# Kernel tuning notes

Measured on AMD Instinct MI355X. Metric: run time of the kernel, lower is better.

## Reference

```python
import jax, jax.numpy as jnp
import numpy as np


def setup_inputs() -> dict:
    key = jax.random.key(0)
    k1, k2, k3, k4 = jax.random.split(key, 4)
    bs, n, f_in, f_out, n_head = 4, 2048, 64, 64, 8
    h = jax.random.normal(k1, (bs, n, f_in), dtype=jnp.float32)
    adj = jnp.ones((bs, n, n), dtype=bool)  # accepted by forward but unused
    # xavier-uniform-like init scales
    w = jax.random.uniform(k2, (n_head, f_in, f_out), dtype=jnp.float32,
                           minval=-1.0, maxval=1.0) * np.sqrt(6.0 / (f_in + f_out))
    a_src = jax.random.uniform(k3, (n_head, f_out, 1), dtype=jnp.float32,
                               minval=-1.0, maxval=1.0) * np.sqrt(6.0 / (f_out + 1))
    a_dst = jax.random.uniform(k4, (n_head, f_out, 1), dtype=jnp.float32,
                               minval=-1.0, maxval=1.0) * np.sqrt(6.0 / (f_out + 1))
    bias_p = jnp.zeros((f_out,), dtype=jnp.float32)
    return {"h": h, "adj": adj, "w": w, "a_src": a_src, "a_dst": a_dst, "bias_p": bias_p}


def reference(h, adj, w, a_src, a_dst, bias_p):
    # h: [b, n, f_in], w: [h, f_in, f_out]
    h_prime = jnp.einsum('bnf,hfo->bhno', h, w)          # [b, h, n, f_out]
    t = jnp.tanh(h_prime)
    attn_src = jnp.einsum('bhno,ho->bhn', t, a_src[..., 0])  # [b, h, n]
    attn_dst = jnp.einsum('bhno,ho->bhn', t, a_dst[..., 0])  # [b, h, n]
    # attn[b,h,i,j] = src[b,h,i] + dst[b,h,j]  (dense; adj unused in original)
    attn = attn_src[..., :, None] + attn_dst[..., None, :]   # [b, h, n, n]
    attn = jnp.where(attn >= 0, attn, 0.2 * attn)            # leaky_relu(0.2)
    attn = jax.nn.softmax(attn, axis=-1)
    # dropout p=0.0 -> identity
    out = jnp.einsum('bhij,bhjo->bhio', attn, h_prime)       # [b, h, n, f_out]
    return out + bias_p
```

## Files before the change

### kernel.cpp

```cpp
#include <hip/hip_runtime.h>
#include <hip/hip_bf16.h>

#define NN 2048
#define FF 64
#define NH 8
#define BDIM 4
#define BH 32

typedef __attribute__((ext_vector_type(8))) short short8;
typedef __attribute__((ext_vector_type(4))) float floatx4;
typedef __attribute__((ext_vector_type(4))) unsigned uint4v;

__device__ __forceinline__ float LDIN(const void* p, size_t i, int b16) {
    return b16 ? __bfloat162float(((const __hip_bfloat16*)p)[i]) : ((const float*)p)[i];
}
__device__ __forceinline__ unsigned packhi(float f0, float f1) {
    return __builtin_amdgcn_perm(__float_as_uint(f1), __float_as_uint(f0), 0x07060302);
}
__device__ __forceinline__ float hitrunc(float x) {
    return __uint_as_float(__float_as_uint(x) & 0xFFFF0000u);
}
__device__ __forceinline__ ushort bf16bits(float v) {
    __hip_bfloat16 b = __float2bfloat16(v);
    return __builtin_bit_cast(ushort, b);
}
__device__ __forceinline__ int SWZ(int row, int col) {
    return row * 64 + ((((col >> 3) ^ (row & 7)) << 3) | (col & 7));
}
__device__ __forceinline__ float fast_tanh(float v) {
    float ex = __expf(2.0f * v);
    return 1.0f - 2.0f * __builtin_amdgcn_rcpf(ex + 1.0f);
}
__device__ __forceinline__ int sniff_b16(const void* h) {
    unsigned word = ((const unsigned*)h)[threadIdx.x & 63];
    unsigned lowexp = (word >> 7) & 0xFFu;
    bool plaus = (lowexp >= 96u && lowexp <= 159u);
    unsigned long long m = __ballot(plaus);
    return (__popcll(m) >= 48) ? 1 : 0;
}

__global__ __launch_bounds__(256) void k_prep(
    const void* __restrict__ h, const void* __restrict__ w,
    ushort* __restrict__ wF, int* __restrict__ flagOut)
{
    const int hd = blockIdx.x, t = threadIdx.x;
    __shared__ int sb16;
    if (t < 64) {
        int f = sniff_b16(h);
        if (t == 0) { sb16 = f; if (hd == 0) flagOut[0] = f; }
    }
    __syncthreads();
    const int b16 = sb16;

#pragma unroll
    for (int g = 0; g < 2; ++g) {
        int gi = t * 2 + g;
        int ml = gi & 15, q = (gi >> 4) & 3, kc = (gi >> 6) & 1, nt = (gi >> 7) & 3;
        int n = nt * 16 + ml, kb = kc * 32 + q * 8;
        size_t off = (size_t)hd * 4096 + ((nt * 2 + kc) * 4 + q) * 128 + ml * 8;
        if (b16) {
            const ushort* wp = (const ushort*)w + (size_t)hd * FF * FF;
            ushort hi[8];
#pragma unroll
            for (int j = 0; j < 8; ++j) hi[j] = wp[(kb + j) * FF + n];
            *(uint4v*)&wF[off] = __builtin_bit_cast(uint4v, *(short8*)hi);
            short8 z = {0, 0, 0, 0, 0, 0, 0, 0};
            *(uint4v*)&wF[off + 32768] = __builtin_bit_cast(uint4v, z);
        } else {
            const float* wp = (const float*)w + (size_t)hd * FF * FF;
            float x[8];
#pragma unroll
            for (int j = 0; j < 8; ++j) x[j] = wp[(kb + j) * FF + n];
            uint4v hv = { packhi(x[0], x[1]), packhi(x[2], x[3]),
                          packhi(x[4], x[5]), packhi(x[6], x[7]) };
            uint4v lv = { packhi(x[0] - hitrunc(x[0]), x[1] - hitrunc(x[1])),
                          packhi(x[2] - hitrunc(x[2]), x[3] - hitrunc(x[3])),
                          packhi(x[4] - hitrunc(x[4]), x[5] - hitrunc(x[5])),
                          packhi(x[6] - hitrunc(x[6]), x[7] - hitrunc(x[7])) };
            *(uint4v*)&wF[off] = hv;
            *(uint4v*)&wF[off + 32768] = lv;
        }
    }
}

__global__ __launch_bounds__(256) void k_proj(
    const void* __restrict__ h, const ushort* __restrict__ wF,
    const void* __restrict__ asrc, const void* __restrict__ adst,
    ushort* __restrict__ hpTt, float* __restrict__ rArr,
    float* __restrict__ edHa, float* __restrict__ edLa)
{
    const int t  = threadIdx.x;
    const int rt = blockIdx.x & 31;
    const int hd = (blockIdx.x >> 5) & 7;
    const int b  = blockIdx.x >> 8;
    const int bh = b * NH + hd;
    const int r0 = rt * 64;

    __shared__ int sb16;
    __shared__ ushort aHi[64 * 64];
    __shared__ ushort aLo[64 * 64];
    __shared__ ushort trans[64 * 64];
    if (t < 64) {
        int f = sniff_b16(h);
        if (t == 0) sb16 = f;
    }
    __syncthreads();
    const int b16 = sb16;

    const int lane = t & 63, wv = t >> 6;
    const int ml = lane & 15, q = lane >> 4;

    if (b16) {
        const ushort* hsrc = (const ushort*)h + (size_t)(b * NN + r0) * FF;
#pragma unroll
        for (int g0 = 0; g0 < 2; ++g0) {
            int g = t + g0 * 256;
            int row = g >> 3, c8 = (g & 7) * 8;
            uint4v u = *(const uint4v*)(hsrc + row * FF + c8);
            *(uint4v*)&aHi[SWZ(row, c8)] = u;
        }
    } else {
        const float* hsrc = (const float*)h + (size_t)(b * NN + r0) * FF;
#pragma unroll
        for (int g0 = 0; g0 < 4; ++g0) {
            int g = t + g0 * 256;
            int row = g >> 4, c4 = (g & 15) * 4;
            floatx4 x = *(const floatx4*)(hsrc + row * FF + c4);
            uint2 hi2 = { packhi(x[0], x[1]), packhi(x[2], x[3]) };
            uint2 lo2 = { packhi(x[0] - hitrunc(x[0]), x[1] - hitrunc(x[1])),
                          packhi(x[2] - hitrunc(x[2]), x[3] - hitrunc(x[3])) };
            *(uint2*)&aHi[SWZ(row, c4)] = hi2;
            *(uint2*)&aLo[SWZ(row, c4)] = lo2;
        }
    }
    __syncthreads();

    short8 ah[2], al[2];
#pragma unroll
    for (int kc = 0; kc < 2; ++kc) {
        ah[kc] = *(const short8*)&aHi[SWZ(wv * 16 + ml, kc * 32 + q * 8)];
        if (!b16) al[kc] = *(const short8*)&aLo[SWZ(wv * 16 + ml, kc * 32 + q * 8)];
    }
    short8 bhf[4][2], blf[4][2];
    const ushort* wfh = wF + (size_t)hd * 4096;
#pragma unroll
    for (int nt = 0; nt < 4; ++nt)
#pragma unroll
        for (int kc = 0; kc < 2; ++kc) {
            size_t off = ((nt * 2 + kc) * 4 + q) * 128 + ml * 8;
            bhf[nt][kc] = __builtin_bit_cast(short8, *(const uint4v*)&wfh[off]);
            if (!b16) blf[nt][kc] = __builtin_bit_cast(short8, *(const uint4v*)&wfh[off + 32768]);
        }

    float aS[4], aD[4];
#pragma unroll
    for (int nt = 0; nt < 4; ++nt) {
        aS[nt] = LDIN(asrc, hd * FF + nt * 16 + ml, b16);
        aD[nt] = LDIN(adst, hd * FF + nt * 16 + ml, b16);
    }

    floatx4 acc[4];
#pragma unroll
    for (int nt = 0; nt < 4; ++nt) {
        floatx4 a = {0.f, 0.f, 0.f, 0.f};
        if (b16) {
#pragma unroll
            for (int kc = 0; kc < 2; ++kc)
                a = __builtin_amdgcn_mfma_f32_16x16x32_bf16(ah[kc], bhf[nt][kc], a, 0, 0, 0);
        } else {
#pragma unroll
            for (int kc = 0; kc < 2; ++kc) {
                a = __builtin_amdgcn_mfma_f32_16x16x32_bf16(ah[kc], bhf[nt][kc], a, 0, 0, 0);
                a = __builtin_amdgcn_mfma_f32_16x16x32_bf16(ah[kc], blf[nt][kc], a, 0, 0, 0);
                a = __builtin_amdgcn_mfma_f32_16x16x32_bf16(al[kc], bhf[nt][kc], a, 0, 0, 0);
            }
        }
        acc[nt] = a;
    }

#pragma unroll
    for (int nt = 0; nt < 4; ++nt) {
        ushort b0 = bf16bits(acc[nt][0]), b1 = bf16bits(acc[nt][1]);
        ushort b2 = bf16bits(acc[nt][2]), b3 = bf16bits(acc[nt][3]);
        uint2 pk = { (unsigned)b0 | ((unsigned)b1 << 16),
                     (unsigned)b2 | ((unsigned)b3 << 16) };
        *(uint2*)&trans[SWZ(nt * 16 + ml, wv * 16 + q * 4)] = pk;
    }

    float ps[4] = {0.f, 0.f, 0.f, 0.f}, pd[4] = {0.f, 0.f, 0.f, 0.f};
#pragma unroll
    for (int nt = 0; nt < 4; ++nt)
#pragma unroll
        for (int reg = 0; reg < 4; ++reg) {
            float tv = fast_tanh(acc[nt][reg]);
            ps[reg] += tv * aS[nt];
            pd[reg] += tv * aD[nt];
        }
#pragma unroll
    for (int msk = 1; msk < 16; msk <<= 1)
#pragma unroll
        for (int reg = 0; reg < 4; ++reg) {
            ps[reg] += __shfl_xor(ps[reg], msk, 64);
            pd[reg] += __shfl_xor(pd[reg], msk, 64);
        }
    if (ml == 0) {
#pragma unroll
        for (int reg = 0; reg < 4; ++reg) {
            int i = bh * NN + r0 + wv * 16 + q * 4 + reg;
            float sv = ps[reg], dv = pd[reg];
            rArr[i] = __expf(-0.8f * sv);
            edHa[i] = __expf(dv);
            edLa[i] = __expf(0.2f * dv);
        }
    }
    __syncthreads();
    {
        const int o = t >> 2, part = (t & 3) * 16;
        uint4v v0 = *(const uint4v*)&trans[SWZ(o, part)];
        uint4v v1 = *(const uint4v*)&trans[SWZ(o, part + 8)];
        ushort* dst = hpTt + (((size_t)bh * 32 + rt) * 64 + o) * 64 + part;
        *(uint4v*)dst = v0;
        *(uint4v*)(dst + 8) = v1;
    }
}

__global__ __launch_bounds__(512) void k_attn(
    const ushort* __restrict__ hpTt, const float* __restrict__ rArr,
    const float* __restrict__ edHa, const float* __restrict__ edLa,
    const void* __restrict__ bias, const int* __restrict__ flag,
    void* __restrict__ out)
{
    const int b16 = flag[0];
    const int t = threadIdx.x;
    const int wv = t >> 6, lane = t & 63;
    const int ml = lane & 15, q = lane >> 4;
    const int bh = blockIdx.x & 31;
    const int i0 = (blockIdx.x >> 5) * 128 + wv * 16;

    __shared__ ushort Bc[4][64 * 64];
    __shared__ __align__(16) float ehS[NN];
    __shared__ __align__(16) float elS[NN];

    ((floatx4*)ehS)[t] = ((const floatx4*)(edHa + bh * NN))[t];
    ((floatx4*)elS)[t] = ((const floatx4*)(edLa + bh * NN))[t];

    const ushort* src = hpTt + (size_t)bh * NN * FF;
    const float r = rArr[bh * NN + i0 + ml];

    const short8 ONESB = {0x3F80, 0x3F80, 0x3F80, 0x3F80,
                          0x3F80, 0x3F80, 0x3F80, 0x3F80};

    floatx4 acc[4];
#pragma unroll
    for (int nt = 0; nt < 4; ++nt) acc[nt] = (floatx4){0.f, 0.f, 0.f, 0.f};
    floatx4 accD = {0.f, 0.f, 0.f, 0.f};

    auto stage = [&](int c) {
        uint4v u = *(const uint4v*)(src + (size_t)c * 4096 + t * 8);
        *(uint4v*)&Bc[c & 3][SWZ(t >> 3, (t & 7) * 8)] = u;
    };

    auto compute = [&](int c) {
        const int j0 = c * 64, buf = c & 3;
#pragma unroll
        for (int ks = 0; ks < 2; ++ks) {
            const int col = ks * 32 + q * 8;
            floatx4 eh0 = *(const floatx4*)&ehS[j0 + col];
            floatx4 eh1 = *(const floatx4*)&ehS[j0 + col + 4];
            floatx4 el0 = *(const floatx4*)&elS[j0 + col];
            floatx4 el1 = *(const floatx4*)&elS[j0 + col + 4];
            short8 Bf[4];
#pragma unroll
            for (int nt = 0; nt < 4; ++nt)
                Bf[nt] = *(const short8*)&Bc[buf][SWZ(nt * 16 + ml, col)];
            float p[8];
#pragma unroll
            for (int j = 0; j < 4; ++j) {
                p[j]     = fmaxf(eh0[j], r * el0[j]);
                p[j + 4] = fmaxf(eh1[j], r * el1[j]);
            }
            uint4v hv = { packhi(p[0], p[1]), packhi(p[2], p[3]),
                          packhi(p[4], p[5]), packhi(p[6], p[7]) };
            short8 PH = __builtin_bit_cast(short8, hv);
#pragma unroll
            for (int nt = 0; nt < 4; ++nt)
                acc[nt] = __builtin_amdgcn_mfma_f32_16x16x32_bf16(PH, Bf[nt], acc[nt], 0, 0, 0);
            accD = __builtin_amdgcn_mfma_f32_16x16x32_bf16(PH, ONESB, accD, 0, 0, 0);
        }
    };

    stage(0); stage(1);
    __syncthreads();
    for (int c = 0; c < 32; c += 2) {
        if (c + 2 < 32) { stage(c + 2); stage(c + 3); }
        compute(c);
        compute(c + 1);
        __syncthreads();
    }

    float biasv[4];
#pragma unroll
    for (int nt = 0; nt < 4; ++nt) biasv[nt] = LDIN(bias, nt * 16 + ml, b16);

#pragma unroll
    for (int reg = 0; reg < 4; ++reg) {
        float inv = 1.0f / accD[reg];
        int i = i0 + q * 4 + reg;
#pragma unroll
        for (int nt = 0; nt < 4; ++nt) {
            float val = acc[nt][reg] * inv + biasv[nt];
            size_t oi = ((size_t)bh * NN + i) * FF + nt * 16 + ml;
            if (b16) ((__hip_bfloat16*)out)[oi] = __float2bfloat16(val);
            else     ((float*)out)[oi] = val;
        }
    }
}

extern "C" void kernel_launch(void* const* d_in, const int* in_sizes, int n_in,
                              void* d_out, int out_size, void* d_ws, size_t ws_size,
                              hipStream_t stream) {
    const void* h    = d_in[0];
    const void* w    = d_in[2];
    const void* asrc = d_in[3];
    const void* adst = d_in[4];
    const void* bias = d_in[5];

    float* ws = (float*)d_ws;
    int*    flag = (int*)ws;
    ushort* hpTt = (ushort*)(ws + 16);
    float*  rArr = (float*)(hpTt + (size_t)BH * NN * FF);
    float*  edHa = rArr + BH * NN;
    float*  edLa = edHa + BH * NN;
    ushort* wF   = (ushort*)(edLa + BH * NN);

    k_prep<<<NH, 256, 0, stream>>>(h, w, wF, flag);
    k_proj<<<BDIM * NH * 32, 256, 0, stream>>>(h, wF, asrc, adst,
                                               hpTt, rArr, edHa, edLa);
    k_attn<<<BH * 16, 512, 0, stream>>>(hpTt, rArr, edHa, edLa,
                                        bias, flag, d_out);
}
```

Baseline: 139.1 us.

## Replace dense attention matmul with sort plus prefix-sum formulation

```diff
diff --git a/kernel.cpp b/kernel.cpp
--- a/kernel.cpp
+++ b/kernel.cpp
@@ -19,10 +19,6 @@
 }
 __device__ __forceinline__ float hitrunc(float x) {
     return __uint_as_float(__float_as_uint(x) & 0xFFFF0000u);
-}
-__device__ __forceinline__ ushort bf16bits(float v) {
-    __hip_bfloat16 b = __float2bfloat16(v);
-    return __builtin_bit_cast(ushort, b);
 }
 __device__ __forceinline__ int SWZ(int row, int col) {
     return row * 64 + ((((col >> 3) ^ (row & 7)) << 3) | (col & 7));
@@ -37,6 +33,16 @@
     bool plaus = (lowexp >= 96u && lowexp <= 159u);
     unsigned long long m = __ballot(plaus);
     return (__popcll(m) >= 48) ? 1 : 0;
+}
+__device__ __forceinline__ unsigned long long packKey(float d, int j) {
+    unsigned u = __float_as_uint(d);
+    u = (u & 0x80000000u) ? ~u : (u | 0x80000000u);
+    return ((unsigned long long)(~u) << 32) | (unsigned)j;
+}
+__device__ __forceinline__ float unpackD(unsigned long long kk) {
+    unsigned u = ~(unsigned)(kk >> 32);
+    u = (u & 0x80000000u) ? (u & 0x7FFFFFFFu) : ~u;
+    return __uint_as_float(u);
 }
 
 __global__ __launch_bounds__(256) void k_prep(
@@ -86,8 +92,8 @@
 __global__ __launch_bounds__(256) void k_proj(
     const void* __restrict__ h, const ushort* __restrict__ wF,
     const void* __restrict__ asrc, const void* __restrict__ adst,
-    ushort* __restrict__ hpTt, float* __restrict__ rArr,
-    float* __restrict__ edHa, float* __restrict__ edLa)
+    float* __restrict__ hpF, float* __restrict__ sArr, float* __restrict__ dArr,
+    float* __restrict__ rArr)
 {
     const int t  = threadIdx.x;
     const int rt = blockIdx.x & 31;
@@ -99,7 +105,7 @@
     __shared__ int sb16;
     __shared__ ushort aHi[64 * 64];
     __shared__ ushort aLo[64 * 64];
-    __shared__ ushort trans[64 * 64];
+    __shared__ float  sF[64 * 68];
     if (t < 64) {
         int f = sniff_b16(h);
         if (t == 0) sb16 = f;
@@ -179,13 +185,10 @@
     }
 
 #pragma unroll
-    for (int nt = 0; nt < 4; ++nt) {
-        ushort b0 = bf16bits(acc[nt][0]), b1 = bf16bits(acc[nt][1]);
-        ushort b2 = bf16bits(acc[nt][2]), b3 = bf16bits(acc[nt][3]);
-        uint2 pk = { (unsigned)b0 | ((unsigned)b1 << 16),
-                     (unsigned)b2 | ((unsigned)b3 << 16) };
-        *(uint2*)&trans[SWZ(nt * 16 + ml, wv * 16 + q * 4)] = pk;
-    }
+    for (int nt = 0; nt < 4; ++nt)
+#pragma unroll
+        for (int reg = 0; reg < 4; ++reg)
+            sF[(wv * 16 + q * 4 + reg) * 68 + nt * 16 + ml] = acc[nt][reg];
 
     float ps[4] = {0.f, 0.f, 0.f, 0.f}, pd[4] = {0.f, 0.f, 0.f, 0.f};
 #pragma unroll
@@ -208,111 +211,175 @@
         for (int reg = 0; reg < 4; ++reg) {
             int i = bh * NN + r0 + wv * 16 + q * 4 + reg;
             float sv = ps[reg], dv = pd[reg];
+            sArr[i] = sv;
+            dArr[i] = dv;
             rArr[i] = __expf(-0.8f * sv);
-            edHa[i] = __expf(dv);
-            edLa[i] = __expf(0.2f * dv);
         }
     }
     __syncthreads();
     {
-        const int o = t >> 2, part = (t & 3) * 16;
-        uint4v v0 = *(const uint4v*)&trans[SWZ(o, part)];
-        uint4v v1 = *(const uint4v*)&trans[SWZ(o, part + 8)];
-        ushort* dst = hpTt + (((size_t)bh * 32 + rt) * 64 + o) * 64 + part;
-        *(uint4v*)dst = v0;
-        *(uint4v*)(dst + 8) = v1;
-    }
-}
-
-__global__ __launch_bounds__(512) void k_attn(
-    const ushort* __restrict__ hpTt, const float* __restrict__ rArr,
-    const float* __restrict__ edHa, const float* __restrict__ edLa,
+        const int row = t >> 2, cs = (t & 3) * 16;
+        const float* sp = &sF[row * 68 + cs];
+        float* dst = hpF + ((size_t)bh * NN + r0 + row) * 64 + cs;
+        *(floatx4*)(dst)      = *(const floatx4*)(sp);
+        *(floatx4*)(dst + 4)  = *(const floatx4*)(sp + 4);
+        *(floatx4*)(dst + 8)  = *(const floatx4*)(sp + 8);
+        *(floatx4*)(dst + 12) = *(const floatx4*)(sp + 12);
+    }
+}
+
+__global__ __launch_bounds__(1024) void k_mid(
+    const float* __restrict__ dArr, const float* __restrict__ hpF,
+    float* __restrict__ SD,
+    float* __restrict__ PreR, float* __restrict__ SufR,
+    float* __restrict__ PreS, float* __restrict__ SufS)
+{
+    const int bh = blockIdx.x, t = threadIdx.x;
+    const int lane = t & 63, wv = t >> 6;
+    __shared__ unsigned long long kp[2048];
+    __shared__ float Teh[64][64];
+    __shared__ float Tel[64][64];
+    __shared__ float TehS[64], TelS[64];
+
+    kp[t]        = packKey(dArr[bh * NN + t], t);
+    kp[t + 1024] = packKey(dArr[bh * NN + t + 1024], t + 1024);
+    __syncthreads();
+
+    for (int k = 2; k <= 2048; k <<= 1) {
+        for (int j = k >> 1; j > 0; j >>= 1) {
+#pragma unroll
+            for (int e = 0; e < 2; ++e) {
+                int a = t + e * 1024, b = a ^ j;
+                if (b > a) {
+                    unsigned long long ka = kp[a], kb = kp[b];
+                    bool up = ((a & k) == 0);
+                    if ((ka > kb) == up) { kp[a] = kb; kp[b] = ka; }
+                }
+            }
+            __syncthreads();
+        }
+    }
+
+    SD[bh * NN + t]        = unpackD(kp[t]);
+    SD[bh * NN + t + 1024] = unpackD(kp[t + 1024]);
+
+#pragma unroll
+    for (int cc = 0; cc < 4; ++cc) {
+        int c = wv * 4 + cc;
+        float teh = 0.f, tel = 0.f, tehs = 0.f, tels = 0.f;
+#pragma unroll 4
+        for (int u = 0; u < 32; ++u) {
+            unsigned long long kk = kp[c * 32 + u];
+            int jj = (int)(kk & 0xFFFFFFFFu);
+            float d = unpackD(kk);
+            float eh = __expf(d), el = __expf(0.2f * d);
+            float hv = hpF[((size_t)bh * NN + jj) * 64 + lane];
+            teh += eh * hv; tel += el * hv; tehs += eh; tels += el;
+        }
+        Teh[c][lane] = teh; Tel[c][lane] = tel;
+        if (lane == 0) { TehS[c] = tehs; TelS[c] = tels; }
+    }
+    __syncthreads();
+
+    if (wv == 0) {
+        float rp = 0.f, rps = 0.f;
+        for (int c = 0; c < 64; ++c) {
+            float tv = Teh[c][lane]; Teh[c][lane] = rp; rp += tv;
+            if (lane == 0) { float ts = TehS[c]; TehS[c] = rps; rps += ts; }
+        }
+        PreR[((size_t)bh * 2049 + 2048) * 64 + lane] = rp;
+        if (lane == 0) PreS[(size_t)bh * 2049 + 2048] = rps;
+    } else if (wv == 1) {
+        float rs = 0.f, rss = 0.f;
+        for (int c = 63; c >= 0; --c) {
+            float tv = Tel[c][lane]; Tel[c][lane] = rs; rs += tv;
+            if (lane == 0) { float ts = TelS[c]; TelS[c] = rss; rss += ts; }
+        }
+        SufR[((size_t)bh * 2049 + 2048) * 64 + lane] = 0.f;
+        if (lane == 0) SufS[(size_t)bh * 2049 + 2048] = 0.f;
+    }
+    __syncthreads();
+
+#pragma unroll
+    for (int cc = 0; cc < 4; ++cc) {
+        int c = wv * 4 + cc;
+        float run = Teh[c][lane];
+        float runs = TehS[c];
+#pragma unroll 4
+        for (int u = 0; u < 32; ++u) {
+            int x = c * 32 + u;
+            unsigned long long kk = kp[x];
+            int jj = (int)(kk & 0xFFFFFFFFu);
+            PreR[((size_t)bh * 2049 + x) * 64 + lane] = run;
+            if (lane == 0) PreS[(size_t)bh * 2049 + x] = runs;
+            float eh = __expf(unpackD(kk));
+            float hv = hpF[((size_t)bh * NN + jj) * 64 + lane];
+            run += eh * hv; runs += eh;
+        }
+        float runb = Tel[c][lane];
+        float runbs = TelS[c];
+#pragma unroll 4
+        for (int u = 31; u >= 0; --u) {
+            int x = c * 32 + u;
+            unsigned long long kk = kp[x];
+            int jj = (int)(kk & 0xFFFFFFFFu);
+            float el = __expf(0.2f * unpackD(kk));
+            float hv = hpF[((size_t)bh * NN + jj) * 64 + lane];
+            runb += el * hv; runbs += el;
+            SufR[((size_t)bh * 2049 + x) * 64 + lane] = runb;
+            if (lane == 0) SufS[(size_t)bh * 2049 + x] = runbs;
+        }
+    }
+}
+
+__global__ __launch_bounds__(128) void k_out(
+    const float* __restrict__ SD, const float* __restrict__ sArr,
+    const float* __restrict__ rArr,
+    const float* __restrict__ PreR, const float* __restrict__ SufR,
+    const float* __restrict__ PreS, const float* __restrict__ SufS,
     const void* __restrict__ bias, const int* __restrict__ flag,
     void* __restrict__ out)
 {
     const int b16 = flag[0];
     const int t = threadIdx.x;
+    const int bh = blockIdx.x >> 4;
+    const int i0 = (blockIdx.x & 15) * 128;
     const int wv = t >> 6, lane = t & 63;
-    const int ml = lane & 15, q = lane >> 4;
-    const int bh = blockIdx.x & 31;
-    const int i0 = (blockIdx.x >> 5) * 128 + wv * 16;
-
-    __shared__ ushort Bc[4][64 * 64];
-    __shared__ __align__(16) float ehS[NN];
-    __shared__ __align__(16) float elS[NN];
-
-    ((floatx4*)ehS)[t] = ((const floatx4*)(edHa + bh * NN))[t];
-    ((floatx4*)elS)[t] = ((const floatx4*)(edLa + bh * NN))[t];
-
-    const ushort* src = hpTt + (size_t)bh * NN * FF;
-    const float r = rArr[bh * NN + i0 + ml];
-
-    const short8 ONESB = {0x3F80, 0x3F80, 0x3F80, 0x3F80,
-                          0x3F80, 0x3F80, 0x3F80, 0x3F80};
-
-    floatx4 acc[4];
-#pragma unroll
-    for (int nt = 0; nt < 4; ++nt) acc[nt] = (floatx4){0.f, 0.f, 0.f, 0.f};
-    floatx4 accD = {0.f, 0.f, 0.f, 0.f};
-
-    auto stage = [&](int c) {
-        uint4v u = *(const uint4v*)(src + (size_t)c * 4096 + t * 8);
-        *(uint4v*)&Bc[c & 3][SWZ(t >> 3, (t & 7) * 8)] = u;
-    };
-
-    auto compute = [&](int c) {
-        const int j0 = c * 64, buf = c & 3;
-#pragma unroll
-        for (int ks = 0; ks < 2; ++ks) {
-            const int col = ks * 32 + q * 8;
-            floatx4 eh0 = *(const floatx4*)&ehS[j0 + col];
-            floatx4 eh1 = *(const floatx4*)&ehS[j0 + col + 4];
-            floatx4 el0 = *(const floatx4*)&elS[j0 + col];
-            floatx4 el1 = *(const floatx4*)&elS[j0 + col + 4];
-            short8 Bf[4];
-#pragma unroll
-            for (int nt = 0; nt < 4; ++nt)
-                Bf[nt] = *(const short8*)&Bc[buf][SWZ(nt * 16 + ml, col)];
-            float p[8];
-#pragma unroll
-            for (int j = 0; j < 4; ++j) {
-                p[j]     = fmaxf(eh0[j], r * el0[j]);
-                p[j + 4] = fmaxf(eh1[j], r * el1[j]);
-            }
-            uint4v hv = { packhi(p[0], p[1]), packhi(p[2], p[3]),
-                          packhi(p[4], p[5]), packhi(p[6], p[7]) };
-            short8 PH = __builtin_bit_cast(short8, hv);
-#pragma unroll
-            for (int nt = 0; nt < 4; ++nt)
-                acc[nt] = __builtin_amdgcn_mfma_f32_16x16x32_bf16(PH, Bf[nt], acc[nt], 0, 0, 0);
-            accD = __builtin_amdgcn_mfma_f32_16x16x32_bf16(PH, ONESB, accD, 0, 0, 0);
-        }
-    };
-
-    stage(0); stage(1);
-    __syncthreads();
-    for (int c = 0; c < 32; c += 2) {
-        if (c + 2 < 32) { stage(c + 2); stage(c + 3); }
-        compute(c);
-        compute(c + 1);
-        __syncthreads();
-    }
-
-    float biasv[4];
-#pragma unroll
-    for (int nt = 0; nt < 4; ++nt) biasv[nt] = LDIN(bias, nt * 16 + ml, b16);
-
-#pragma unroll
-    for (int reg = 0; reg < 4; ++reg) {
-        float inv = 1.0f / accD[reg];
-        int i = i0 + q * 4 + reg;
-#pragma unroll
-        for (int nt = 0; nt < 4; ++nt) {
-            float val = acc[nt][reg] * inv + biasv[nt];
-            size_t oi = ((size_t)bh * NN + i) * FF + nt * 16 + ml;
-            if (b16) ((__hip_bfloat16*)out)[oi] = __float2bfloat16(val);
-            else     ((float*)out)[oi] = val;
-        }
+
+    __shared__ float sdL[2048];
+    __shared__ int   cntS[128];
+    __shared__ float rS[128];
+#pragma unroll
+    for (int g = 0; g < 4; ++g)
+        ((floatx4*)sdL)[t + g * 128] = ((const floatx4*)(SD + bh * NN))[t + g * 128];
+    __syncthreads();
+
+    {
+        int i = i0 + wv * 64 + lane;
+        float thr = -sArr[bh * NN + i];
+        int lo = 0, hi = 2048;
+        while (lo < hi) {
+            int m = (lo + hi) >> 1;
+            if (sdL[m] >= thr) lo = m + 1; else hi = m;
+        }
+        cntS[wv * 64 + lane] = lo;
+        rS[wv * 64 + lane] = rArr[bh * NN + i];
+    }
+    __syncthreads();
+
+    float biasv = LDIN(bias, lane, b16);
+    for (int u = 0; u < 64; ++u) {
+        int iu = wv * 64 + u;
+        int cnt = cntS[iu];
+        float rr = rS[iu];
+        size_t ro = ((size_t)bh * 2049 + cnt) * 64 + lane;
+        float pre = PreR[ro], suf = SufR[ro];
+        float pres = PreS[(size_t)bh * 2049 + cnt];
+        float sufs = SufS[(size_t)bh * 2049 + cnt];
+        float val = (pre + rr * suf) / (pres + rr * sufs) + biasv;
+        size_t oi = ((size_t)bh * NN + i0 + iu) * 64 + lane;
+        if (b16) ((__hip_bfloat16*)out)[oi] = __float2bfloat16(val);
+        else     ((float*)out)[oi] = val;
     }
 }
 
@@ -327,15 +394,21 @@
 
     float* ws = (float*)d_ws;
     int*    flag = (int*)ws;
-    ushort* hpTt = (ushort*)(ws + 16);
-    float*  rArr = (float*)(hpTt + (size_t)BH * NN * FF);
-    float*  edHa = rArr + BH * NN;
-    float*  edLa = edHa + BH * NN;
-    ushort* wF   = (ushort*)(edLa + BH * NN);
+    float*  hpF  = ws + 16;
+    float*  sArr = hpF + (size_t)BH * NN * FF;
+    float*  dArr = sArr + BH * NN;
+    float*  rArr = dArr + BH * NN;
+    float*  SD   = rArr + BH * NN;
+    float*  PreR = SD + BH * NN;
+    float*  SufR = PreR + (size_t)BH * 2049 * FF;
+    float*  PreS = SufR + (size_t)BH * 2049 * FF;
+    float*  SufS = PreS + (size_t)BH * 2049;
+    ushort* wF   = (ushort*)(SufS + (size_t)BH * 2049);
 
     k_prep<<<NH, 256, 0, stream>>>(h, w, wF, flag);
     k_proj<<<BDIM * NH * 32, 256, 0, stream>>>(h, wF, asrc, adst,
-                                               hpTt, rArr, edHa, edLa);
-    k_attn<<<BH * 16, 512, 0, stream>>>(hpTt, rArr, edHa, edLa,
-                                        bias, flag, d_out);
-}
+                                               hpF, sArr, dArr, rArr);
+    k_mid<<<BH, 1024, 0, stream>>>(dArr, hpF, SD, PreR, SufR, PreS, SufS);
+    k_out<<<BH * 16, 128, 0, stream>>>(SD, sArr, rArr, PreR, SufR, PreS, SufS,
+                                       bias, flag, d_out);
+}
```

Result: slower. 248.6 us (+78.7%).
